# Kernel tuning notes

Measured on AMD Instinct MI355X. Metric: run time of the kernel, lower is better.

Reference implementation:

```python
import jax, jax.numpy as jnp
import numpy as np

MARGIN = 0.3
N, D = 8192, 1024
NUM_IDS = 751

def setup_inputs() -> dict:
    key = jax.random.key(0)
    k1, k2 = jax.random.split(key)
    inputs = jax.random.normal(k1, (N, D), dtype=jnp.float32)
    targets = jax.random.randint(k2, (N,), 0, NUM_IDS, dtype=jnp.int64)
    return {"inputs": inputs, "targets": targets}

def reference(inputs, targets):
    # sim[i,j] = <x_i, x_j>
    sim = jnp.matmul(inputs, inputs.T)  # [N, N]
    same = targets[:, None] == targets[None, :]  # [N, N] bool
    # positives: same label AND sim < 1 -> contribute (1 - sim)
    pos_mask = same & (sim < 1.0)
    pos_loss = jnp.sum(jnp.where(pos_mask, 1.0 - sim, 0.0), axis=1)  # [N]
    # negatives: different label AND sim > margin -> contribute sim
    neg_mask = (~same) & (sim > MARGIN)
    neg_loss = jnp.sum(jnp.where(neg_mask, sim, 0.0), axis=1)  # [N]
    n = inputs.shape[0]
    return jnp.sum(pos_loss + neg_loss) / n
```

## Files before the change

kernel.cpp:

```cpp
#include <hip/hip_runtime.h>
#include <stdint.h>

typedef int v4i __attribute__((ext_vector_type(4)));

#define NROWS 8192
#define DIM   1024
#define BK    128
#define NKT   (DIM / BK)
#define MARGIN 0.3f
#define QSCALE 22.0f
#define QINV   (1.0f / (QSCALE * QSCALE))

#define GLOAD_LDS16(gp, lp)                                                    \
  __builtin_amdgcn_global_load_lds(                                            \
      (const __attribute__((address_space(1))) void*)(gp),                     \
      (__attribute__((address_space(3))) void*)(lp), 16, 0, 0)

__global__ __launch_bounds__(256) void cvt_f32_i8(const float* __restrict__ in,
                                                  uint8_t* __restrict__ out,
                                                  float* __restrict__ loss) {
  if (blockIdx.x == 0 && threadIdx.x == 0) loss[0] = 0.0f;
  size_t i = ((size_t)blockIdx.x * 256 + threadIdx.x) * 16;
#define Q1(x_) (((int)rintf(fminf(fmaxf((x_) * QSCALE, -127.f), 127.f))) & 255)
#define Q4(v_) ((unsigned)(Q1(v_.x) | (Q1(v_.y) << 8) | (Q1(v_.z) << 16) | (Q1(v_.w) << 24)))
  float4 v0 = *(const float4*)(in + i);
  float4 v1 = *(const float4*)(in + i + 4);
  float4 v2 = *(const float4*)(in + i + 8);
  float4 v3 = *(const float4*)(in + i + 12);
  uint4 p;
  p.x = Q4(v0); p.y = Q4(v1); p.z = Q4(v2); p.w = Q4(v3);
  *(uint4*)(out + i) = p;
#undef Q1
#undef Q4
}

__global__ __launch_bounds__(256, 3) void gram_loss(const uint8_t* __restrict__ A8,
                                                    const int* __restrict__ targets,
                                                    float* __restrict__ out) {
  __shared__ uint8_t As[128 * 128];
  __shared__ uint8_t Bs[128 * 128];
  __shared__ int tRow[128];
  __shared__ int tCol[128];
  __shared__ float wsum[4];

  const int pos = (blockIdx.x & 7) * 260 + (blockIdx.x >> 3);
  int q = 0, pre = 0;
  if (pos >= 136)  { q = 1; pre = 136; }
  if (pos >= 392)  { q = 2; pre = 392; }
  if (pos >= 648)  { q = 3; pre = 648; }
  if (pos >= 904)  { q = 4; pre = 904; }
  if (pos >= 1040) { q = 5; pre = 1040; }
  if (pos >= 1296) { q = 6; pre = 1296; }
  if (pos >= 1552) { q = 7; pre = 1552; }
  if (pos >= 1688) { q = 8; pre = 1688; }
  if (pos >= 1944) { q = 9; pre = 1944; }
  const int r  = pos - pre;
  const int Si = (q >= 4) + (q >= 7) + (q >= 9);
  const int Sj = Si + (q - (Si * 4 - (Si * (Si - 1)) / 2));
  int li, lj;
  if (Si == Sj) {
    li = (r>=16)+(r>=31)+(r>=45)+(r>=58)+(r>=70)+(r>=81)+(r>=91)+(r>=100)
       + (r>=108)+(r>=115)+(r>=121)+(r>=126)+(r>=130)+(r>=133)+(r>=135);
    lj = li + (r - (li * (33 - li)) / 2);
  } else {
    li = r >> 4;
    lj = r & 15;
  }
  const int bi = Si * 16 + li;
  const int bj = Sj * 16 + lj;

  const int iBase = bi * 128;
  const int jBase = bj * 128;

  const int tid  = threadIdx.x;
  const int wave = tid >> 6;
  const int lane = tid & 63;

  if (tid < 128) tRow[tid] = targets[iBase + tid];
  else           tCol[tid - 128] = targets[jBase + tid - 128];

  const int lrow = lane >> 3;
  const int cg   = (lane & 7) ^ lrow;
  const uint8_t* gA = A8 + (size_t)(iBase + wave * 32 + lrow) * DIM + cg * 16;
  const uint8_t* gB = A8 + (size_t)(jBase + wave * 32 + lrow) * DIM + cg * 16;
  uint8_t* lA = &As[wave * 32 * 128];
  uint8_t* lB = &Bs[wave * 32 * 128];

  const int m0 = (wave >> 1) * 64;
  const int n0 = (wave & 1) * 64;
  const int fr = lane & 15;
  const int h  = lane >> 4;
  const int r7 = fr & 7;
  const int s0 = ((h    ) ^ r7) * 16;
  const int s1 = ((h + 4) ^ r7) * 16;

  v4i acc[4][4] = {};

#define STAGE(kt_)                                                             \
  { const int kO_ = (kt_) * BK;                                                \
    _Pragma("unroll")                                                          \
    for (int l = 0; l < 4; ++l)                                                \
      GLOAD_LDS16(gA + (size_t)(l * 8) * DIM + kO_, lA + l * 8 * 128);         \
    _Pragma("unroll")                                                          \
    for (int l = 0; l < 4; ++l)                                                \
      GLOAD_LDS16(gB + (size_t)(l * 8) * DIM + kO_, lB + l * 8 * 128); }

  STAGE(0);
  asm volatile("s_waitcnt vmcnt(0)" ::: "memory");
  __builtin_amdgcn_s_barrier();

  for (int kt = 0; kt < NKT; ++kt) {
    v4i a0[4], b0[4], a1[4], b1[4];
#pragma unroll
    for (int mi = 0; mi < 4; ++mi)
      a0[mi] = *(const v4i*)&As[(m0 + mi * 16 + fr) * 128 + s0];
#pragma unroll
    for (int ni = 0; ni < 4; ++ni)
      b0[ni] = *(const v4i*)&Bs[(n0 + ni * 16 + fr) * 128 + s0];
#pragma unroll
    for (int mi = 0; mi < 4; ++mi)
      a1[mi] = *(const v4i*)&As[(m0 + mi * 16 + fr) * 128 + s1];
#pragma unroll
    for (int ni = 0; ni < 4; ++ni)
      b1[ni] = *(const v4i*)&Bs[(n0 + ni * 16 + fr) * 128 + s1];
    asm volatile("s_waitcnt lgkmcnt(0)" ::: "memory");
    __builtin_amdgcn_s_barrier();
    if (kt + 1 < NKT) STAGE(kt + 1);
    __builtin_amdgcn_sched_barrier(0);
#pragma unroll
    for (int mi = 0; mi < 4; ++mi)
#pragma unroll
      for (int ni = 0; ni < 4; ++ni) {
        acc[mi][ni] = __builtin_amdgcn_mfma_i32_16x16x64_i8(
            a0[mi], b0[ni], acc[mi][ni], 0, 0, 0);
        acc[mi][ni] = __builtin_amdgcn_mfma_i32_16x16x64_i8(
            a1[mi], b1[ni], acc[mi][ni], 0, 0, 0);
      }
    __builtin_amdgcn_sched_barrier(0);
    asm volatile("s_waitcnt vmcnt(0)" ::: "memory");
    __builtin_amdgcn_s_barrier();
  }
#undef STAGE

  const int col = lane & 15;
  const int rquad = (lane >> 4) * 4;
  float lsum = 0.0f;
#pragma unroll
  for (int ni = 0; ni < 4; ++ni) {
    const int tj = tCol[n0 + ni * 16 + col];
#pragma unroll
    for (int mi = 0; mi < 4; ++mi) {
#pragma unroll
      for (int r2 = 0; r2 < 4; ++r2) {
        float s = (float)acc[mi][ni][r2] * QINV;
        int ti = tRow[m0 + mi * 16 + rquad + r2];
        lsum += (ti == tj) ? (s < 1.0f ? 1.0f - s : 0.0f)
                           : (s > MARGIN ? s : 0.0f);
      }
    }
  }
  if (bi != bj) lsum *= 2.0f;

#pragma unroll
  for (int off = 32; off > 0; off >>= 1) lsum += __shfl_down(lsum, off, 64);
  if (lane == 0) wsum[wave] = lsum;
  __syncthreads();
  if (tid == 0)
    atomicAdd(out, (wsum[0] + wsum[1] + wsum[2] + wsum[3]) * (1.0f / (float)NROWS));
}

extern "C" void kernel_launch(void* const* d_in, const int* in_sizes, int n_in,
                              void* d_out, int out_size, void* d_ws, size_t ws_size,
                              hipStream_t stream) {
  const float* x = (const float*)d_in[0];
  const int* targets = (const int*)d_in[1];
  float* out = (float*)d_out;
  uint8_t* x8 = (uint8_t*)d_ws;

  cvt_f32_i8<<<2048, 256, 0, stream>>>(x, x8, out);
  gram_loss<<<2080, 256, 0, stream>>>(x8, targets, out);
}
```

Before: 127.5 us.

## Load MFMA operands directly from global memory instead of staging through LDS

Removes the LDS staging buffers, the async global-to-LDS copies and the per-iteration barriers. Each wave now loads its A and B fragments straight from global memory into registers every k-step. This drops shared-memory traffic and synchronisation, but every wave re-fetches data that other waves in the block share, which raises L2/L1 traffic. Loads also no longer overlap with compute through explicit staging and depend on the compiler's scheduling.

```diff
diff --git a/kernel.cpp b/kernel.cpp
--- a/kernel.cpp
+++ b/kernel.cpp
@@ -10,11 +10,6 @@
 #define MARGIN 0.3f
 #define QSCALE 22.0f
 #define QINV   (1.0f / (QSCALE * QSCALE))
-
-#define GLOAD_LDS16(gp, lp)                                                    \
-  __builtin_amdgcn_global_load_lds(                                            \
-      (const __attribute__((address_space(1))) void*)(gp),                     \
-      (__attribute__((address_space(3))) void*)(lp), 16, 0, 0)
 
 __global__ __launch_bounds__(256) void cvt_f32_i8(const float* __restrict__ in,
                                                   uint8_t* __restrict__ out,
@@ -37,8 +32,6 @@
 __global__ __launch_bounds__(256, 3) void gram_loss(const uint8_t* __restrict__ A8,
                                                     const int* __restrict__ targets,
                                                     float* __restrict__ out) {
-  __shared__ uint8_t As[128 * 128];
-  __shared__ uint8_t Bs[128 * 128];
   __shared__ int tRow[128];
   __shared__ int tCol[128];
   __shared__ float wsum[4];
@@ -78,55 +71,35 @@
 
   if (tid < 128) tRow[tid] = targets[iBase + tid];
   else           tCol[tid - 128] = targets[jBase + tid - 128];
-
-  const int lrow = lane >> 3;
-  const int cg   = (lane & 7) ^ lrow;
-  const uint8_t* gA = A8 + (size_t)(iBase + wave * 32 + lrow) * DIM + cg * 16;
-  const uint8_t* gB = A8 + (size_t)(jBase + wave * 32 + lrow) * DIM + cg * 16;
-  uint8_t* lA = &As[wave * 32 * 128];
-  uint8_t* lB = &Bs[wave * 32 * 128];
+  __syncthreads();
 
   const int m0 = (wave >> 1) * 64;
   const int n0 = (wave & 1) * 64;
   const int fr = lane & 15;
   const int h  = lane >> 4;
-  const int r7 = fr & 7;
-  const int s0 = ((h    ) ^ r7) * 16;
-  const int s1 = ((h + 4) ^ r7) * 16;
+
+  const uint8_t* pA0 = A8 + (size_t)(iBase + m0 +  0 + fr) * DIM + h * 16;
+  const uint8_t* pA1 = A8 + (size_t)(iBase + m0 + 16 + fr) * DIM + h * 16;
+  const uint8_t* pA2 = A8 + (size_t)(iBase + m0 + 32 + fr) * DIM + h * 16;
+  const uint8_t* pA3 = A8 + (size_t)(iBase + m0 + 48 + fr) * DIM + h * 16;
+  const uint8_t* pB0 = A8 + (size_t)(jBase + n0 +  0 + fr) * DIM + h * 16;
+  const uint8_t* pB1 = A8 + (size_t)(jBase + n0 + 16 + fr) * DIM + h * 16;
+  const uint8_t* pB2 = A8 + (size_t)(jBase + n0 + 32 + fr) * DIM + h * 16;
+  const uint8_t* pB3 = A8 + (size_t)(jBase + n0 + 48 + fr) * DIM + h * 16;
 
   v4i acc[4][4] = {};
 
-#define STAGE(kt_)                                                             \
-  { const int kO_ = (kt_) * BK;                                                \
-    _Pragma("unroll")                                                          \
-    for (int l = 0; l < 4; ++l)                                                \
-      GLOAD_LDS16(gA + (size_t)(l * 8) * DIM + kO_, lA + l * 8 * 128);         \
-    _Pragma("unroll")                                                          \
-    for (int l = 0; l < 4; ++l)                                                \
-      GLOAD_LDS16(gB + (size_t)(l * 8) * DIM + kO_, lB + l * 8 * 128); }
-
-  STAGE(0);
-  asm volatile("s_waitcnt vmcnt(0)" ::: "memory");
-  __builtin_amdgcn_s_barrier();
-
   for (int kt = 0; kt < NKT; ++kt) {
-    v4i a0[4], b0[4], a1[4], b1[4];
-#pragma unroll
-    for (int mi = 0; mi < 4; ++mi)
-      a0[mi] = *(const v4i*)&As[(m0 + mi * 16 + fr) * 128 + s0];
-#pragma unroll
-    for (int ni = 0; ni < 4; ++ni)
-      b0[ni] = *(const v4i*)&Bs[(n0 + ni * 16 + fr) * 128 + s0];
-#pragma unroll
-    for (int mi = 0; mi < 4; ++mi)
-      a1[mi] = *(const v4i*)&As[(m0 + mi * 16 + fr) * 128 + s1];
-#pragma unroll
-    for (int ni = 0; ni < 4; ++ni)
-      b1[ni] = *(const v4i*)&Bs[(n0 + ni * 16 + fr) * 128 + s1];
-    asm volatile("s_waitcnt lgkmcnt(0)" ::: "memory");
-    __builtin_amdgcn_s_barrier();
-    if (kt + 1 < NKT) STAGE(kt + 1);
-    __builtin_amdgcn_sched_barrier(0);
+    const int kO = kt * BK;
+    v4i a0[4], a1[4], b0[4], b1[4];
+    a0[0] = *(const v4i*)(pA0 + kO);      a1[0] = *(const v4i*)(pA0 + kO + 64);
+    a0[1] = *(const v4i*)(pA1 + kO);      a1[1] = *(const v4i*)(pA1 + kO + 64);
+    a0[2] = *(const v4i*)(pA2 + kO);      a1[2] = *(const v4i*)(pA2 + kO + 64);
+    a0[3] = *(const v4i*)(pA3 + kO);      a1[3] = *(const v4i*)(pA3 + kO + 64);
+    b0[0] = *(const v4i*)(pB0 + kO);      b1[0] = *(const v4i*)(pB0 + kO + 64);
+    b0[1] = *(const v4i*)(pB1 + kO);      b1[1] = *(const v4i*)(pB1 + kO + 64);
+    b0[2] = *(const v4i*)(pB2 + kO);      b1[2] = *(const v4i*)(pB2 + kO + 64);
+    b0[3] = *(const v4i*)(pB3 + kO);      b1[3] = *(const v4i*)(pB3 + kO + 64);
 #pragma unroll
     for (int mi = 0; mi < 4; ++mi)
 #pragma unroll
@@ -136,11 +109,7 @@
         acc[mi][ni] = __builtin_amdgcn_mfma_i32_16x16x64_i8(
             a1[mi], b1[ni], acc[mi][ni], 0, 0, 0);
       }
-    __builtin_amdgcn_sched_barrier(0);
-    asm volatile("s_waitcnt vmcnt(0)" ::: "memory");
-    __builtin_amdgcn_s_barrier();
   }
-#undef STAGE
 
   const int col = lane & 15;
   const int rquad = (lane >> 4) * 4;
```

After: 228.1 us. 78.9% more time.
